# Kernel tuning notes

Hardware: AMD Instinct MI355X
Metric: run time of the kernel (lower is better)

## Reference

```python
import math
import jax, jax.numpy as jnp
import numpy as np

B, T = 2, 2048
D_MODEL, D_HEAD = 2048, 128
N_Q, N_KV = 16, 4
QPG = N_Q // N_KV  # queries per kv group
ROPE_BASE = 10000.0
YARN_SCALE = 4.0
ORIG_MAX_LEN = 4096
BETA_FAST, BETA_SLOW = 32.0, 1.0
RMS_EPS = 1.1920929e-07  # torch.finfo(float32).eps (nn.RMSNorm default)


def _yarn_inv_freq():
    inv = 1.0 / ROPE_BASE ** (np.arange(0, D_HEAD, 2, dtype=np.float32) / D_HEAD)
    wavelengths = 2.0 * math.pi / inv
    low_wavelen = ORIG_MAX_LEN / BETA_SLOW
    high_wavelen = ORIG_MAX_LEN / BETA_FAST
    gamma = np.clip((low_wavelen - wavelengths) / (low_wavelen - high_wavelen), 0.0, 1.0)
    return (gamma * inv + (1.0 - gamma) * inv / YARN_SCALE).astype(np.float32)

INV_FREQ = jnp.asarray(_yarn_inv_freq())  # (D_HEAD//2,) constant buffer
MSCALE = 0.1 * math.log(YARN_SCALE) + 1.0
ATTN_SCALE = 1.0 / (MSCALE * math.sqrt(D_HEAD))


def _rms_norm(x, w):
    # normalize over last dim (d_head), learnable per-dim weight
    return x * jax.lax.rsqrt(jnp.mean(x * x, axis=-1, keepdims=True) + RMS_EPS) * w


def _apply_rope(x):
    # x: (..., T, d_head)
    t = jnp.arange(x.shape[-2], dtype=jnp.float32)
    freqs = jnp.outer(t, INV_FREQ)                 # (T, d/2)
    emb = jnp.concatenate([freqs, freqs], axis=-1)  # (T, d)
    cos, sin = jnp.cos(emb), jnp.sin(emb)
    half = x.shape[-1] // 2
    x_rot = jnp.concatenate([-x[..., half:], x[..., :half]], axis=-1)
    return x * cos + x_rot * sin


def setup_inputs() -> dict:
    key = jax.random.key(0)
    ks = jax.random.split(key, 5)
    x = jax.random.normal(ks[0], (B, T, D_MODEL), dtype=jnp.float32)
    w_scale = 0.02
    Wq = jax.random.normal(ks[1], (D_MODEL, N_Q * D_HEAD), dtype=jnp.float32) * w_scale
    Wkv = jax.random.normal(ks[2], (D_MODEL, 2 * N_KV * D_HEAD), dtype=jnp.float32) * w_scale
    Wo = jax.random.normal(ks[3], (N_Q * D_HEAD, D_MODEL), dtype=jnp.float32) * w_scale
    q_norm_w = jnp.ones((D_HEAD,), dtype=jnp.float32)
    k_norm_w = jnp.ones((D_HEAD,), dtype=jnp.float32)
    return {"x": x, "Wq": Wq, "Wkv": Wkv, "Wo": Wo,
            "q_norm_w": q_norm_w, "k_norm_w": k_norm_w}


def reference(x, Wq, Wkv, Wo, q_norm_w, k_norm_w):
    b, t, _ = x.shape
    # projections
    q = (x @ Wq).reshape(b, t, QPG, N_KV, D_HEAD).transpose(0, 2, 3, 1, 4)  # (b,qpg,g,t,d)
    kv = x @ Wkv
    k, v = jnp.split(kv, 2, axis=-1)
    k = k.reshape(b, t, N_KV, D_HEAD).transpose(0, 2, 1, 3)  # (b,g,t,d)
    v = v.reshape(b, t, N_KV, D_HEAD).transpose(0, 2, 1, 3)  # (b,g,t,d)
    # RMSNorm + YaRN RoPE on q,k (math done in float32 as in source)
    q = _apply_rope(_rms_norm(q, q_norm_w))
    k = _apply_rope(_rms_norm(k, k_norm_w))
    # GQA replication: head index h = qpg*N_KV + g (matches source rearrange/reshape)
    q = q.reshape(b, N_Q, t, D_HEAD)
    k = jnp.broadcast_to(k[:, None], (b, QPG, N_KV, t, D_HEAD)).reshape(b, N_Q, t, D_HEAD)
    v = jnp.broadcast_to(v[:, None], (b, QPG, N_KV, t, D_HEAD)).reshape(b, N_Q, t, D_HEAD)
    # causal SDPA with custom scale
    scores = jnp.einsum('bhtd,bhsd->bhts', q, k) * ATTN_SCALE
    causal = jnp.tril(jnp.ones((t, t), dtype=bool))
    scores = jnp.where(causal, scores, jnp.finfo(scores.dtype).min)
    probs = jax.nn.softmax(scores, axis=-1)
    attn = jnp.einsum('bhts,bhsd->bhtd', probs, v)
    out = attn.transpose(0, 2, 1, 3).reshape(b, t, N_Q * D_HEAD)
    return out @ Wo
```

## Files before the change

kernel.cpp:

```cpp
#include <hip/hip_runtime.h>
#include <cmath>

typedef float f32x4 __attribute__((ext_vector_type(4)));
typedef float f32x16 __attribute__((ext_vector_type(16)));
typedef __bf16 bf16x8 __attribute__((ext_vector_type(8)));

#define DEV static __device__ __forceinline__

DEV unsigned short f2bf(float f) {
  unsigned int u = __builtin_bit_cast(unsigned int, f);
  u += 0x7FFFu + ((u >> 16) & 1u);
  return (unsigned short)(u >> 16);
}
DEV float bf2f(unsigned short h) {
  unsigned int u = ((unsigned int)h) << 16;
  return __builtin_bit_cast(float, u);
}
DEV unsigned int cvtpk(float lo, float hi) {
  unsigned int r;
  asm("v_cvt_pk_bf16_f32 %0, %1, %2" : "=v"(r) : "v"(lo), "v"(hi));
  return r;
}
DEV f32x4 mfma16(bf16x8 a, bf16x8 b, f32x4 c) {
  return __builtin_amdgcn_mfma_f32_16x16x32_bf16(a, b, c, 0, 0, 0);
}
DEV f32x16 mfma32(bf16x8 a, bf16x8 b, f32x16 c) {
  return __builtin_amdgcn_mfma_f32_32x32x16_bf16(a, b, c, 0, 0, 0);
}
DEV void dma16(const void* g, void* l) {
  __builtin_amdgcn_global_load_lds(
      (const __attribute__((address_space(1))) void*)(uintptr_t)g,
      (__attribute__((address_space(3))) void*)(unsigned int)(uintptr_t)l,
      16, 0, 0);
}

constexpr int T_SEQ = 2048;

__global__ __launch_bounds__(256) void build_rope(float2* __restrict__ rope) {
  int gid = blockIdx.x * 256 + threadIdx.x;
  if (gid >= T_SEQ * 64) return;
  int t = gid >> 6, i = gid & 63;
  double inv = pow(10000.0, -((double)(2 * i)) / 128.0);
  double wl = 6.283185307179586 / inv;
  double gm = (4096.0 - wl) / (4096.0 - 128.0);
  gm = gm < 0.0 ? 0.0 : (gm > 1.0 ? 1.0 : gm);
  float f = (float)(gm * inv + (1.0 - gm) * inv * 0.25);
  float th = (float)t * f;
  float s, c;
  sincosf(th, &s, &c);
  rope[gid] = make_float2(c, s);
}

__global__ __launch_bounds__(256) void cvt_f32_bf16(const float4* __restrict__ in,
                                                    ushort* __restrict__ out, int n4) {
  int i = blockIdx.x * 256 + threadIdx.x;
  if (i >= n4) return;
  float4 v = in[i];
  unsigned int lo = (unsigned int)f2bf(v.x) | ((unsigned int)f2bf(v.y) << 16);
  unsigned int hi = (unsigned int)f2bf(v.z) | ((unsigned int)f2bf(v.w) << 16);
  int row = i >> 9;
  int e = (i * 4) & 2047;
  size_t o = ((size_t)row << 11) + (size_t)(e ^ ((row & 7) << 3));
  *(uint2*)(out + o) = make_uint2(lo, hi);
}

__global__ __launch_bounds__(256) void tconv(const float* __restrict__ in,
                                             ushort* __restrict__ out, int R, int C) {
  __shared__ ushort tile[64][65];
  int c0 = blockIdx.x * 64, r0 = blockIdx.y * 64;
  int j = threadIdx.x & 63, i0 = threadIdx.x >> 6;
#pragma unroll
  for (int ii = 0; ii < 16; ++ii) {
    int i = i0 + ii * 4;
    tile[i][j] = f2bf(in[(size_t)(r0 + i) * C + c0 + j]);
  }
  __syncthreads();
#pragma unroll
  for (int ii = 0; ii < 16; ++ii) {
    int jr = i0 + ii * 4;
    out[(size_t)(c0 + jr) * R + ((r0 + j) ^ ((jr & 7) << 3))] = tile[j][jr];
  }
}

template <int OUT_BF16>
__global__ __launch_bounds__(256) void gemm_bt(const ushort* __restrict__ A,
                                               const ushort* __restrict__ Bt,
                                               void* __restrict__ Cv,
                                               int M, int N, int K) {
  __shared__ ushort lA[128 * 64];
  __shared__ ushort lB[128 * 64];
  const int tid = threadIdx.x;
  const int lane = tid & 63;
  const int w = tid >> 6;
  const int m0 = blockIdx.y * 128;
  const int n0 = blockIdx.x * 128;
  const int wm = (w >> 1) << 6;
  const int wn = (w & 1) << 6;

  f32x4 acc[4][4] = {};

  const size_t K2 = (size_t)K * 2;
  const char* Ab = (const char*)A + (size_t)m0 * K2;
  const char* Bb = (const char*)Bt + (size_t)n0 * K2;
  const int drow = w * 32 + (lane >> 3);
  const int dcb = (lane & 7) * 16;

  for (int k0 = 0; k0 < K; k0 += 64) {
#pragma unroll
    for (int ii = 0; ii < 4; ++ii) {
      const int off = w * 4096 + ii * 1024;
      const size_t gofs = (size_t)(drow + ii * 8) * K2 + (size_t)k0 * 2 + dcb;
      dma16(Ab + gofs, (char*)lA + off);
      dma16(Bb + gofs, (char*)lB + off);
    }
    __syncthreads();
#pragma unroll
    for (int kc = 0; kc < 2; ++kc) {
      bf16x8 a[4], bb[4];
#pragma unroll
      for (int mt = 0; mt < 4; ++mt) {
        int row = wm + mt * 16 + (lane & 15);
        int byo = kc * 64 + ((lane >> 4) << 4);
        a[mt] = *(const bf16x8*)((const char*)lA + row * 128 + (byo ^ ((row & 7) << 4)));
      }
#pragma unroll
      for (int nt = 0; nt < 4; ++nt) {
        int row = wn + nt * 16 + (lane & 15);
        int byo = kc * 64 + ((lane >> 4) << 4);
        bb[nt] = *(const bf16x8*)((const char*)lB + row * 128 + (byo ^ ((row & 7) << 4)));
      }
#pragma unroll
      for (int mt = 0; mt < 4; ++mt)
#pragma unroll
        for (int nt = 0; nt < 4; ++nt)
          acc[mt][nt] = mfma16(a[mt], bb[nt], acc[mt][nt]);
    }
    __syncthreads();
  }

  const int rr = (lane >> 4) << 2;
  const int cc = lane & 15;
  if (OUT_BF16) {
    ushort* C = (ushort*)Cv;
#pragma unroll
    for (int mt = 0; mt < 4; ++mt)
#pragma unroll
      for (int nt = 0; nt < 4; ++nt)
#pragma unroll
        for (int j = 0; j < 4; ++j) {
          int r = m0 + wm + mt * 16 + rr + j;
          int c = n0 + wn + nt * 16 + cc;
          C[(size_t)r * N + c] = f2bf(acc[mt][nt][j]);
        }
  } else {
    float* C = (float*)Cv;
#pragma unroll
    for (int mt = 0; mt < 4; ++mt)
#pragma unroll
      for (int nt = 0; nt < 4; ++nt)
#pragma unroll
        for (int j = 0; j < 4; ++j) {
          int r = m0 + wm + mt * 16 + rr + j;
          int c = n0 + wn + nt * 16 + cc;
          C[(size_t)r * N + c] = acc[mt][nt][j];
        }
  }
}

__global__ __launch_bounds__(256) void norm_rope(const ushort* __restrict__ qkv,
                                                 const float* __restrict__ qw,
                                                 const float* __restrict__ kw,
                                                 const float2* __restrict__ rope,
                                                 ushort* __restrict__ qout,
                                                 ushort* __restrict__ kout,
                                                 float q_scale) {
  const int w = threadIdx.x >> 6, lane = threadIdx.x & 63;
  const int vi = blockIdx.x * 4 + w;
  const ushort* src;
  const float* wt;
  ushort* dst;
  float extra;
  int t, bb;
  if (vi < 65536) {
    int row = vi >> 4, H = vi & 15;
    bb = row >> 11;
    t = row & 2047;
    src = qkv + (size_t)row * 3072 + H * 128 + lane * 2;
    wt = qw;
    extra = q_scale;
    dst = qout + ((size_t)(bb * 16 + H) * T_SEQ + t) * 128 + lane * 2;
  } else {
    int vi2 = vi - 65536;
    int row = vi2 >> 2, gg = vi2 & 3;
    bb = row >> 11;
    t = row & 2047;
    src = qkv + (size_t)row * 3072 + 2048 + gg * 128 + lane * 2;
    wt = kw;
    extra = 1.f;
    dst = kout + ((size_t)(bb * 4 + gg) * T_SEQ + t) * 128 +
          ((lane * 2) ^ ((t & 15) << 3));
  }
  float x0 = bf2f(src[0]), x1 = bf2f(src[1]);
  float ss = x0 * x0 + x1 * x1;
#pragma unroll
  for (int d = 1; d < 64; d <<= 1) ss += __shfl_xor(ss, d, 64);
  float sc = rsqrtf(ss * (1.f / 128.f) + 1.1920929e-7f);
  float w0 = wt[lane * 2], w1 = wt[lane * 2 + 1];
  float xn0 = x0 * sc * w0, xn1 = x1 * sc * w1;
  float p0 = __shfl_xor(xn0, 32, 64), p1 = __shfl_xor(xn1, 32, 64);
  float r0 = lane < 32 ? -p0 : p0;
  float r1 = lane < 32 ? -p1 : p1;
  int i0 = (lane * 2) & 63;
  float2 cs0 = rope[t * 64 + i0];
  float2 cs1 = rope[t * 64 + i0 + 1];
  float o0 = (xn0 * cs0.x + r0 * cs0.y) * extra;
  float o1 = (xn1 * cs1.x + r1 * cs1.y) * extra;
  unsigned int pk = (unsigned int)f2bf(o0) | ((unsigned int)f2bf(o1) << 16);
  *(unsigned int*)dst = pk;
}

__global__ __launch_bounds__(256) void tv_kernel(const ushort* __restrict__ qkv,
                                                 ushort* __restrict__ vt) {
  __shared__ ushort tile[64][65];
  int t0 = blockIdx.x * 64;
  int y = blockIdx.y;
  int dh = y & 1, bg = y >> 1;
  int bb = bg >> 2, g = bg & 3;
  int j = threadIdx.x & 63, i0 = threadIdx.x >> 6;
#pragma unroll
  for (int ii = 0; ii < 16; ++ii) {
    int i = i0 + ii * 4;
    tile[i][j] = qkv[(size_t)(bb * T_SEQ + t0 + i) * 3072 + 2560 + g * 128 + dh * 64 + j];
  }
  __syncthreads();
#pragma unroll
  for (int ii = 0; ii < 16; ++ii) {
    int jr = i0 + ii * 4;
    vt[((size_t)bg * 128 + dh * 64 + jr) * T_SEQ + t0 + j] = tile[j][jr];
  }
}

#define MKPA(P, B)                                                      \
  ({                                                                    \
    unsigned X1 = cvtpk(P[B + 0], P[B + 1]);                            \
    unsigned X2 = cvtpk(P[B + 2], P[B + 3]);                            \
    unsigned Y1 = cvtpk(P[B + 4], P[B + 5]);                            \
    unsigned Y2 = cvtpk(P[B + 6], P[B + 7]);                            \
    asm("v_permlane32_swap_b32 %0, %1" : "+v"(X1), "+v"(Y1));           \
    asm("v_permlane32_swap_b32 %0, %1" : "+v"(X2), "+v"(Y2));           \
    uint4 u4 = {X1, X2, Y1, Y2};                                        \
    __builtin_bit_cast(bf16x8, u4);                                     \
  })

__global__ __launch_bounds__(128, 2) void attn_fwd(const ushort* __restrict__ qh,
                                                   const ushort* __restrict__ kh,
                                                   const ushort* __restrict__ vt,
                                                   ushort* __restrict__ o) {
  const int f = blockIdx.x;
  const int half = f >> 9, c = f & 511;
  const int kk = c >> 5, bh = c & 31;
  const int qt = half ? kk : (31 - kk);
  const int b = bh >> 4, H = bh & 15;
  const int g = H & 3;
  const int tid = threadIdx.x, lane = tid & 63, w = tid >> 6;
  const int hi = lane >> 5;
  const int ql = lane & 31;
  const int qbase = qt * 64 + 32 * w;

  __shared__ ushort lK[2][32 * 128];
  __shared__ ushort lV[2][32 * 128];

  bf16x8 qf[8];
  {
    const ushort* qb = qh + ((size_t)(b * 16 + H) * T_SEQ + qbase + ql) * 128 + 8 * hi;
#pragma unroll
    for (int cc = 0; cc < 8; ++cc) qf[cc] = *(const bf16x8*)(qb + 16 * cc);
  }

  f32x16 oacc[4] = {};
  float mrow = -INFINITY, lrow = 0.f;

  const char* kpl = (const char*)(kh + (size_t)(b * 4 + g) * T_SEQ * 128);
  const char* vpl = (const char*)(vt + (size_t)(b * 4 + g) * 128 * T_SEQ);

  auto stage = [&](int kt, int bi) {
#pragma unroll
    for (int ii = 0; ii < 4; ++ii) {
      const int off = w * 4096 + ii * 1024;
      dma16(kpl + (size_t)kt * 8192 + off + lane * 16, (char*)lK[bi] + off);
      const int r = 16 * w + 4 * ii + (lane >> 4);
      const int cb = (lane & 15) * 16;
      const int cp = cb ^ ((r & 15) << 4);
      const int d = r + 32 * (cp >> 6);
      dma16(vpl + (size_t)d * (T_SEQ * 2) + (size_t)kt * 64 + (cp & 63),
            (char*)lV[bi] + off);
    }
  };

  stage(0, 0);

  const int swK = (ql & 15) << 4;
  const int kmax = 2 * qt + 1;
  const int kact = 2 * qt + w;

  for (int kt = 0; kt <= kmax; ++kt) {
    const int cur = kt & 1;
    if (kt < kmax) {
      stage(kt + 1, cur ^ 1);
      asm volatile("s_waitcnt vmcnt(8)" ::: "memory");
    } else {
      asm volatile("s_waitcnt vmcnt(0)" ::: "memory");
    }
    __builtin_amdgcn_s_barrier();
    __builtin_amdgcn_sched_barrier(0);

    if (kt <= kact) {
      const char* lKc = (const char*)lK[cur];
      const char* lVc = (const char*)lV[cur];

      f32x16 s = {};
      __builtin_amdgcn_s_setprio(1);
#pragma unroll
      for (int cc = 0; cc < 8; ++cc) {
        bf16x8 kf = *(const bf16x8*)(lKc + ql * 256 + ((32 * cc + 16 * hi) ^ swK));
        s = mfma32(kf, qf[cc], s);
      }
      __builtin_amdgcn_s_setprio(0);

      if (kt == kact) {
        const int q = qbase + ql;
        const int kvb = kt * 32 + 4 * hi;
#pragma unroll
        for (int r = 0; r < 16; ++r) {
          const int kv = kvb + (r & 3) + 8 * (r >> 2);
          if (kv > q) s[r] = -3.0e38f;
        }
      }

      float tm[8];
#pragma unroll
      for (int r = 0; r < 8; ++r) tm[r] = fmaxf(s[r], s[r + 8]);
      float pm = fmaxf(fmaxf(fmaxf(tm[0], tm[1]), fmaxf(tm[2], tm[3])),
                       fmaxf(fmaxf(tm[4], tm[5]), fmaxf(tm[6], tm[7])));
      pm = fmaxf(pm, __shfl_xor(pm, 32, 64));

      float mn = mrow;
      if (!__all(pm <= mrow + 11.5417f)) {
        mn = fmaxf(mrow, pm);
        float rsc = exp2f(mrow - mn);
        mrow = mn;
        lrow *= rsc;
#pragma unroll
        for (int r = 0; r < 16; ++r) {
          float rv = __shfl(rsc, (r & 3) + 8 * (r >> 2) + 4 * hi, 64);
#pragma unroll
          for (int n = 0; n < 4; ++n) oacc[n][r] *= rv;
        }
      }

      f32x16 p;
#pragma unroll
      for (int r = 0; r < 16; ++r) p[r] = exp2f(s[r] - mn);
      float ta[8];
#pragma unroll
      for (int r = 0; r < 8; ++r) ta[r] = p[r] + p[r + 8];
      float ps = ((ta[0] + ta[1]) + (ta[2] + ta[3])) + ((ta[4] + ta[5]) + (ta[6] + ta[7]));
      ps += __shfl_xor(ps, 32, 64);
      lrow += ps;

      bf16x8 pa0 = MKPA(p, 0), pa1 = MKPA(p, 8);

      __builtin_amdgcn_s_setprio(1);
      const char* vb = lVc + ql * 256;
#pragma unroll
      for (int n = 0; n < 4; ++n) {
        bf16x8 vf0 = *(const bf16x8*)(vb + ((n * 64 + 16 * hi) ^ swK));
        bf16x8 vf1 = *(const bf16x8*)(vb + ((n * 64 + 32 + 16 * hi) ^ swK));
        oacc[n] = mfma32(pa0, vf0, oacc[n]);
        oacc[n] = mfma32(pa1, vf1, oacc[n]);
      }
      __builtin_amdgcn_s_setprio(0);
    }

    __builtin_amdgcn_sched_barrier(0);
    __builtin_amdgcn_s_barrier();
  }

  float linv = 1.f / lrow;
#pragma unroll
  for (int r = 0; r < 16; ++r) {
    const int qrr = (r & 3) + 8 * (r >> 2) + 4 * hi;
    float iv = __shfl(linv, qrr, 64);
    const int row = qbase + qrr;
    const size_t base = (size_t)(b * T_SEQ + row) * 2048;
    const int sw = (row & 7) << 3;
#pragma unroll
    for (int n = 0; n < 4; ++n) {
      int col = H * 128 + n * 32 + ql;
      o[base + (col ^ sw)] = f2bf(oacc[n][r] * iv);
    }
  }
}

extern "C" void kernel_launch(void* const* d_in, const int* in_sizes, int n_in,
                              void* d_out, int out_size, void* d_ws, size_t ws_size,
                              hipStream_t stream) {
  (void)in_sizes; (void)n_in; (void)out_size; (void)ws_size;
  const float* x = (const float*)d_in[0];
  const float* Wq = (const float*)d_in[1];
  const float* Wkv = (const float*)d_in[2];
  const float* Wo = (const float*)d_in[3];
  const float* qnw = (const float*)d_in[4];
  const float* knw = (const float*)d_in[5];
  float* out = (float*)d_out;
  char* ws = (char*)d_ws;

  ushort* xb = (ushort*)(ws);
  ushort* wqkv = (ushort*)(ws + 16777216);
  ushort* wot = (ushort*)(ws + 29360128);
  ushort* qkvraw = (ushort*)(ws + 37748736);
  ushort* kh = (ushort*)(ws + 62914560);
  ushort* vtp = (ushort*)(ws + 67108864);
  float2* rope = (float2*)(ws + 71303168);
  ushort* qh = xb;
  ushort* attnb = qkvraw;

  float attn_scale = 1.0f / ((0.1f * logf(4.0f) + 1.0f) * sqrtf(128.0f));
  float q_scale = attn_scale * 1.44269504f;

  build_rope<<<512, 256, 0, stream>>>(rope);
  cvt_f32_bf16<<<8192, 256, 0, stream>>>((const float4*)x, xb, 2097152);
  tconv<<<dim3(32, 32), 256, 0, stream>>>(Wq, wqkv, 2048, 2048);
  tconv<<<dim3(16, 32), 256, 0, stream>>>(Wkv, wqkv + (size_t)2048 * 2048, 2048, 1024);
  tconv<<<dim3(32, 32), 256, 0, stream>>>(Wo, wot, 2048, 2048);
  gemm_bt<1><<<dim3(24, 32), 256, 0, stream>>>(xb, wqkv, qkvraw, 4096, 3072, 2048);
  norm_rope<<<20480, 256, 0, stream>>>(qkvraw, qnw, knw, rope, qh, kh, q_scale);
  tv_kernel<<<dim3(32, 16), 256, 0, stream>>>(qkvraw, vtp);
  attn_fwd<<<1024, 128, 0, stream>>>(qh, kh, vtp, attnb);
  gemm_bt<0><<<dim3(16, 32), 256, 0, stream>>>(attnb, wot, out, 4096, 2048, 2048);
}
```

Baseline: 237.6 us.

## Enlarge attention tiles to 128 queries by 128 keys with single-buffered staging

The attention kernel now uses 256-thread blocks (4 waves) covering 128 query rows and processes 128-key tiles per iteration in four 32-key sub-blocks. The grid is halved to 512 blocks. Each staged K/V tile is now reused by more query rows, and there are fewer barriers and softmax rescale checks per key. In exchange the double buffering is gone: each iteration waits on vmcnt(0) and issues the next load only after compute, so load latency is no longer overlapped within a block, and LDS use per block rises.

```diff
diff --git a/kernel.cpp b/kernel.cpp
--- a/kernel.cpp
+++ b/kernel.cpp
@@ -252,23 +252,23 @@
     __builtin_bit_cast(bf16x8, u4);                                     \
   })
 
-__global__ __launch_bounds__(128, 2) void attn_fwd(const ushort* __restrict__ qh,
+__global__ __launch_bounds__(256, 2) void attn_fwd(const ushort* __restrict__ qh,
                                                    const ushort* __restrict__ kh,
                                                    const ushort* __restrict__ vt,
                                                    ushort* __restrict__ o) {
   const int f = blockIdx.x;
-  const int half = f >> 9, c = f & 511;
+  const int half = f >> 8, c = f & 255;
   const int kk = c >> 5, bh = c & 31;
-  const int qt = half ? kk : (31 - kk);
+  const int qt = half ? kk : (15 - kk);
   const int b = bh >> 4, H = bh & 15;
   const int g = H & 3;
   const int tid = threadIdx.x, lane = tid & 63, w = tid >> 6;
   const int hi = lane >> 5;
   const int ql = lane & 31;
-  const int qbase = qt * 64 + 32 * w;
-
-  __shared__ ushort lK[2][32 * 128];
-  __shared__ ushort lV[2][32 * 128];
+  const int qbase = qt * 128 + 32 * w;
+
+  __shared__ ushort lK[128 * 128];
+  __shared__ ushort lV[32 * 512];
 
   bf16x8 qf[8];
   {
@@ -283,107 +283,122 @@
   const char* kpl = (const char*)(kh + (size_t)(b * 4 + g) * T_SEQ * 128);
   const char* vpl = (const char*)(vt + (size_t)(b * 4 + g) * 128 * T_SEQ);
 
-  auto stage = [&](int kt, int bi) {
-#pragma unroll
-    for (int ii = 0; ii < 4; ++ii) {
-      const int off = w * 4096 + ii * 1024;
-      dma16(kpl + (size_t)kt * 8192 + off + lane * 16, (char*)lK[bi] + off);
-      const int r = 16 * w + 4 * ii + (lane >> 4);
-      const int cb = (lane & 15) * 16;
-      const int cp = cb ^ ((r & 15) << 4);
-      const int d = r + 32 * (cp >> 6);
-      dma16(vpl + (size_t)d * (T_SEQ * 2) + (size_t)kt * 64 + (cp & 63),
-            (char*)lV[bi] + off);
+  auto stage = [&](int kt) {
+#pragma unroll
+    for (int ii = 0; ii < 8; ++ii) {
+      const int koff = (w * 8 + ii) * 1024;
+      const int krow = (w * 8 + ii) * 4 + (lane >> 4);
+      dma16(kpl + (size_t)(kt * 128 + krow) * 256 + (lane & 15) * 16,
+            (char*)lK + koff);
+      const int r = w * 8 + ii;
+      const int n = lane >> 4;
+      const int cp = ((lane & 15) * 16) ^ ((r & 15) << 4);
+      dma16(vpl + (size_t)(r + 32 * n) * (T_SEQ * 2) + (size_t)kt * 256 + cp,
+            (char*)lV + r * 1024);
     }
   };
 
-  stage(0, 0);
-
-  const int swK = (ql & 15) << 4;
-  const int kmax = 2 * qt + 1;
-  const int kact = 2 * qt + w;
-
-  for (int kt = 0; kt <= kmax; ++kt) {
-    const int cur = kt & 1;
-    if (kt < kmax) {
-      stage(kt + 1, cur ^ 1);
-      asm volatile("s_waitcnt vmcnt(8)" ::: "memory");
-    } else {
-      asm volatile("s_waitcnt vmcnt(0)" ::: "memory");
-    }
+  stage(0);
+
+  const int swz = (ql & 15) << 4;
+
+  for (int kt = 0; kt <= qt; ++kt) {
+    asm volatile("s_waitcnt vmcnt(0)" ::: "memory");
     __builtin_amdgcn_s_barrier();
     __builtin_amdgcn_sched_barrier(0);
 
-    if (kt <= kact) {
-      const char* lKc = (const char*)lK[cur];
-      const char* lVc = (const char*)lV[cur];
-
-      f32x16 s = {};
-      __builtin_amdgcn_s_setprio(1);
-#pragma unroll
-      for (int cc = 0; cc < 8; ++cc) {
-        bf16x8 kf = *(const bf16x8*)(lKc + ql * 256 + ((32 * cc + 16 * hi) ^ swK));
-        s = mfma32(kf, qf[cc], s);
-      }
-      __builtin_amdgcn_s_setprio(0);
-
-      if (kt == kact) {
-        const int q = qbase + ql;
-        const int kvb = kt * 32 + 4 * hi;
-#pragma unroll
-        for (int r = 0; r < 16; ++r) {
-          const int kv = kvb + (r & 3) + 8 * (r >> 2);
-          if (kv > q) s[r] = -3.0e38f;
+    const int nsub = (kt == qt) ? (w + 1) : 4;
+
+    f32x16 s[4];
+    __builtin_amdgcn_s_setprio(1);
+#pragma unroll
+    for (int sub = 0; sub < 4; ++sub) {
+      if (sub < nsub) {
+        const char* kb = (const char*)lK + (sub * 32 + ql) * 256;
+        f32x16 a = {};
+#pragma unroll
+        for (int cc = 0; cc < 8; ++cc) {
+          bf16x8 kf = *(const bf16x8*)(kb + ((32 * cc + 16 * hi) ^ swz));
+          a = mfma32(kf, qf[cc], a);
         }
-      }
-
-      float tm[8];
-#pragma unroll
-      for (int r = 0; r < 8; ++r) tm[r] = fmaxf(s[r], s[r + 8]);
-      float pm = fmaxf(fmaxf(fmaxf(tm[0], tm[1]), fmaxf(tm[2], tm[3])),
-                       fmaxf(fmaxf(tm[4], tm[5]), fmaxf(tm[6], tm[7])));
-      pm = fmaxf(pm, __shfl_xor(pm, 32, 64));
-
-      float mn = mrow;
-      if (!__all(pm <= mrow + 11.5417f)) {
-        mn = fmaxf(mrow, pm);
-        float rsc = exp2f(mrow - mn);
-        mrow = mn;
-        lrow *= rsc;
-#pragma unroll
-        for (int r = 0; r < 16; ++r) {
-          float rv = __shfl(rsc, (r & 3) + 8 * (r >> 2) + 4 * hi, 64);
-#pragma unroll
-          for (int n = 0; n < 4; ++n) oacc[n][r] *= rv;
+        s[sub] = a;
+      }
+    }
+    __builtin_amdgcn_s_setprio(0);
+
+    if (kt == qt) {
+      const int sub = w;
+#pragma unroll
+      for (int r = 0; r < 16; ++r) {
+        const int kv = 4 * hi + (r & 3) + 8 * (r >> 2);
+        if (kv > ql) s[sub][r] = -3.0e38f;
+      }
+    }
+
+    float pm = -INFINITY;
+#pragma unroll
+    for (int sub = 0; sub < 4; ++sub) {
+      if (sub < nsub) {
+        float tm[8];
+#pragma unroll
+        for (int r = 0; r < 8; ++r) tm[r] = fmaxf(s[sub][r], s[sub][r + 8]);
+        float v = fmaxf(fmaxf(fmaxf(tm[0], tm[1]), fmaxf(tm[2], tm[3])),
+                        fmaxf(fmaxf(tm[4], tm[5]), fmaxf(tm[6], tm[7])));
+        pm = fmaxf(pm, v);
+      }
+    }
+    pm = fmaxf(pm, __shfl_xor(pm, 32, 64));
+
+    float mn = mrow;
+    if (!__all(pm <= mrow + 11.5417f)) {
+      mn = fmaxf(mrow, pm);
+      float rsc = exp2f(mrow - mn);
+      mrow = mn;
+      lrow *= rsc;
+#pragma unroll
+      for (int r = 0; r < 16; ++r) {
+        float rv = __shfl(rsc, (r & 3) + 8 * (r >> 2) + 4 * hi, 64);
+#pragma unroll
+        for (int n = 0; n < 4; ++n) oacc[n][r] *= rv;
+      }
+    }
+
+    float ps = 0.f;
+#pragma unroll
+    for (int sub = 0; sub < 4; ++sub) {
+      if (sub < nsub) {
+#pragma unroll
+        for (int r = 0; r < 16; ++r) s[sub][r] = exp2f(s[sub][r] - mn);
+        float ta[8];
+#pragma unroll
+        for (int r = 0; r < 8; ++r) ta[r] = s[sub][r] + s[sub][r + 8];
+        ps += ((ta[0] + ta[1]) + (ta[2] + ta[3])) + ((ta[4] + ta[5]) + (ta[6] + ta[7]));
+      }
+    }
+    ps += __shfl_xor(ps, 32, 64);
+    lrow += ps;
+
+    __builtin_amdgcn_s_setprio(1);
+#pragma unroll
+    for (int sub = 0; sub < 4; ++sub) {
+      if (sub < nsub) {
+        bf16x8 paA = MKPA(s[sub], 0), paB = MKPA(s[sub], 8);
+        const char* vb = (const char*)lV + ql * 1024;
+        const int jA = 2 * sub, jB = 2 * sub + 1;
+#pragma unroll
+        for (int n = 0; n < 4; ++n) {
+          bf16x8 vfA = *(const bf16x8*)(vb + n * 256 + ((jA * 32 + 16 * hi) ^ swz));
+          bf16x8 vfB = *(const bf16x8*)(vb + n * 256 + ((jB * 32 + 16 * hi) ^ swz));
+          oacc[n] = mfma32(paA, vfA, oacc[n]);
+          oacc[n] = mfma32(paB, vfB, oacc[n]);
         }
       }
-
-      f32x16 p;
-#pragma unroll
-      for (int r = 0; r < 16; ++r) p[r] = exp2f(s[r] - mn);
-      float ta[8];
-#pragma unroll
-      for (int r = 0; r < 8; ++r) ta[r] = p[r] + p[r + 8];
-      float ps = ((ta[0] + ta[1]) + (ta[2] + ta[3])) + ((ta[4] + ta[5]) + (ta[6] + ta[7]));
-      ps += __shfl_xor(ps, 32, 64);
-      lrow += ps;
-
-      bf16x8 pa0 = MKPA(p, 0), pa1 = MKPA(p, 8);
-
-      __builtin_amdgcn_s_setprio(1);
-      const char* vb = lVc + ql * 256;
-#pragma unroll
-      for (int n = 0; n < 4; ++n) {
-        bf16x8 vf0 = *(const bf16x8*)(vb + ((n * 64 + 16 * hi) ^ swK));
-        bf16x8 vf1 = *(const bf16x8*)(vb + ((n * 64 + 32 + 16 * hi) ^ swK));
-        oacc[n] = mfma32(pa0, vf0, oacc[n]);
-        oacc[n] = mfma32(pa1, vf1, oacc[n]);
-      }
-      __builtin_amdgcn_s_setprio(0);
-    }
+    }
+    __builtin_amdgcn_s_setprio(0);
 
     __builtin_amdgcn_sched_barrier(0);
     __builtin_amdgcn_s_barrier();
+    if (kt < qt) stage(kt + 1);
   }
 
   float linv = 1.f / lrow;
@@ -436,6 +451,6 @@
   gemm_bt<1><<<dim3(24, 32), 256, 0, stream>>>(xb, wqkv, qkvraw, 4096, 3072, 2048);
   norm_rope<<<20480, 256, 0, stream>>>(qkvraw, qnw, knw, rope, qh, kh, q_scale);
   tv_kernel<<<dim3(32, 16), 256, 0, stream>>>(qkvraw, vtp);
-  attn_fwd<<<1024, 128, 0, stream>>>(qh, kh, vtp, attnb);
+  attn_fwd<<<512, 256, 0, stream>>>(qh, kh, vtp, attnb);
   gemm_bt<0><<<dim3(16, 32), 256, 0, stream>>>(attnb, wot, out, 4096, 2048, 2048);
 }
```

New measurement: 307.0 us. +29.2%, slower.
